# Performance work log

Measured on AMD Instinct MI355X. Metric: run time of the kernel, lower is better.

Reference implementation:

```python
import jax, jax.numpy as jnp
import numpy as np

NUM_ITERATIONS = 3


def _squash_elementwise(s):
    # Faithful to original: squared_norm summed over trailing axis of size 1
    # => elementwise squash v = s^2 * s / ((1 + s^2) * sqrt(s^2))
    sq = s * s
    return sq * s / ((1.0 + sq) * jnp.sqrt(sq))


def setup_inputs() -> dict:
    key = jax.random.key(0)
    k1, k2 = jax.random.split(key)
    B, R, C, O, I = 256, 1152, 10, 16, 8
    x = jax.random.normal(k1, (B, R, I), dtype=jnp.float32)
    W = jax.random.normal(k2, (R, C, O, I), dtype=jnp.float32)
    return {"x": x, "W": W}


def reference(x, W):
    # x: (B, R, I); W: (R, C, O, I)
    R, C, O, I = W.shape
    # u_hat[b,r,c,o] = sum_i W[r,c,o,i] * x[b,r,i]   (matmul W @ x per route/capsule)
    u_hat = jnp.einsum('rcoi,bri->brco', W, x)  # (B, R, C, O)
    b_ij = jnp.zeros((R, C), dtype=x.dtype)  # batch-shared routing logits
    v = None
    for it in range(NUM_ITERATIONS):
        c_ij = jax.nn.softmax(b_ij, axis=0)  # softmax over routes (dim=1 in torch)
        s_j = jnp.einsum('rc,brco->bco', c_ij, u_hat)  # weighted sum over routes
        v = _squash_elementwise(s_j)  # (B, C, O)
        if it < NUM_ITERATIONS - 1:
            # agreement a[b,r,c] = u_hat[b,r,c,:] . v[b,c,:]
            a_ij = jnp.einsum('brco,bco->brc', u_hat, v)
            b_ij = b_ij + a_ij.mean(axis=0)  # mean over batch, batch-shared update
    return v[..., None]  # (B, C, O, 1) matches v_j.squeeze(1)
```

## Files before the change

### kernel.cpp

```cpp
#include <hip/hip_runtime.h>

static constexpr int B_ = 256;
static constexpr int R_ = 1152;
static constexpr int C_ = 10;
static constexpr int O_ = 16;
static constexpr int I_ = 8;
static constexpr int SCO = C_ * O_;
static constexpr int K_ = R_ * I_;
static constexpr int NB = 256;

typedef short bf16x8 __attribute__((ext_vector_type(8)));
typedef float f32x4  __attribute__((ext_vector_type(4)));

__device__ __forceinline__ unsigned short f2bf(float f) {
  union { float f; unsigned int u; } c; c.f = f;
  const unsigned int u = c.u;
  return (unsigned short)((u + 0x7fffu + ((u >> 16) & 1u)) >> 16);
}
__device__ __forceinline__ float bf2f(unsigned short h) {
  union { unsigned int u; float f; } c; c.u = ((unsigned int)h) << 16; return c.f;
}

#define FLAG_IDX(b)    ((b) * 16)
#define REQ_IDX(k)     (4096 + (k) * 16)
#define ACK_IDX(e)     (4224 + ((e) - 1) * 16)
#define GO_IDX(k)      (4352 + (k) * 16)
#define RESP_IDX(e, x) (4480 + (((e) - 1) * 8 + (x)) * 16)
#define NBLK_IDX(x)    (5120 + (x) * 16)

__device__ __forceinline__ void gsync(unsigned int* bar, unsigned int epoch,
                                      unsigned int myxcd) {
  __syncthreads();
  const int bx = blockIdx.x, t = threadIdx.x;
  if (bx == 0) {
    if (t == 0)
      __hip_atomic_store(&bar[FLAG_IDX(0)], epoch,
                         __ATOMIC_RELAXED, __HIP_MEMORY_SCOPE_AGENT);
    if (t < 256) {
      int guard = 0;
      while (__hip_atomic_load(&bar[FLAG_IDX(t)],
                               __ATOMIC_RELAXED, __HIP_MEMORY_SCOPE_AGENT) < epoch) {
        __builtin_amdgcn_s_sleep(4);
        if (++guard > (1 << 18)) break;
      }
    }
    __syncthreads();
    if (t == 0) {
      for (int k2 = 0; k2 < 8; ++k2)
        __hip_atomic_store(&bar[REQ_IDX(k2)], epoch,
                           __ATOMIC_RELAXED, __HIP_MEMORY_SCOPE_AGENT);
      const unsigned oldr = __hip_atomic_fetch_add(&bar[RESP_IDX(epoch, myxcd)], 1u,
                              __ATOMIC_RELAXED, __HIP_MEMORY_SCOPE_AGENT);
      if (oldr == 0)
        __hip_atomic_fetch_add(&bar[ACK_IDX(epoch)], 1u,
                               __ATOMIC_RELEASE, __HIP_MEMORY_SCOPE_AGENT);
      unsigned nx = 0;
      for (int x2 = 0; x2 < 8; ++x2)
        nx += (__hip_atomic_load(&bar[NBLK_IDX(x2)],
                 __ATOMIC_RELAXED, __HIP_MEMORY_SCOPE_AGENT) > 0u) ? 1u : 0u;
      int guard = 0;
      while (__hip_atomic_load(&bar[ACK_IDX(epoch)],
                               __ATOMIC_RELAXED, __HIP_MEMORY_SCOPE_AGENT) < nx) {
        __builtin_amdgcn_s_sleep(4);
        if (++guard > (1 << 18)) break;
      }
      __builtin_amdgcn_fence(__ATOMIC_RELEASE, "agent");
      for (int k2 = 0; k2 < 8; ++k2)
        __hip_atomic_store(&bar[GO_IDX(k2)], epoch,
                           __ATOMIC_RELAXED, __HIP_MEMORY_SCOPE_AGENT);
    }
  } else {
    if (t == 0) {
      __hip_atomic_store(&bar[FLAG_IDX(bx)], epoch,
                         __ATOMIC_RELAXED, __HIP_MEMORY_SCOPE_AGENT);
      unsigned int* rq = &bar[REQ_IDX(bx & 7)];
      int guard = 0;
      while (__hip_atomic_load(rq, __ATOMIC_RELAXED,
                               __HIP_MEMORY_SCOPE_AGENT) < epoch) {
        __builtin_amdgcn_s_sleep(8);
        if (++guard > (1 << 17)) break;
      }
      const unsigned oldr = __hip_atomic_fetch_add(&bar[RESP_IDX(epoch, myxcd)], 1u,
                              __ATOMIC_RELAXED, __HIP_MEMORY_SCOPE_AGENT);
      if (oldr == 0)
        __hip_atomic_fetch_add(&bar[ACK_IDX(epoch)], 1u,
                               __ATOMIC_RELEASE, __HIP_MEMORY_SCOPE_AGENT);
      unsigned int* g = &bar[GO_IDX(bx & 7)];
      guard = 0;
      while (__hip_atomic_load(g, __ATOMIC_RELAXED,
                               __HIP_MEMORY_SCOPE_AGENT) < epoch) {
        __builtin_amdgcn_s_sleep(16);
        if (++guard > (1 << 17)) break;
      }
    }
  }
  __syncthreads();
  asm volatile("" ::: "memory");
}

__device__ __forceinline__ void gemm_phase(
    int git, const unsigned short* __restrict__ xb,
    const unsigned short* __restrict__ wraw, const float* __restrict__ eX,
    float* __restrict__ Z, unsigned short* __restrict__ vbw,
    float* __restrict__ out, unsigned char* smem,
    int bx, int t, int w, int mrow, int quad) {
  float* sred = (float*)smem;
  float* szed = (float*)(smem + 16384);
  float* e_lds = (float*)(smem + 20480);
  const int xcd = bx & 7, j = bx >> 3;
  const int mtile = (xcd >> 1) * 4 + j / 5;
  const int c = (xcd & 1) * 5 + j % 5;
  const int m0 = mtile * 16;
  if (git > 0) {
    for (int idx = t; idx < 1152; idx += 512) e_lds[idx] = eX[c * 1152 + idx];
    if (t < 10) szed[t] = atomicAdd(&Z[git * 10 + t], 0.0f);
    __syncthreads();
  }
  const unsigned short* ap = xb + (size_t)(m0 + mrow) * K_ + w * 1152 + quad * 8;
  const unsigned short* bp = wraw + ((size_t)(w * 144 + quad) * C_ + c) * 128 + mrow * 8;
  f32x4 acc = {0.0f, 0.0f, 0.0f, 0.0f};
  if (git == 0) {
#pragma unroll 6
    for (int kk = 0; kk < 36; ++kk) {
      const bf16x8 a = *(const bf16x8*)(ap + kk * 32);
      const bf16x8 b = *(const bf16x8*)(bp + (size_t)kk * 5120);
      acc = __builtin_amdgcn_mfma_f32_16x16x32_bf16(a, b, acc, 0, 0, 0);
    }
  } else {
#pragma unroll 6
    for (int kk = 0; kk < 36; ++kk) {
      const bf16x8 a = *(const bf16x8*)(ap + kk * 32);
      const bf16x8 braw = *(const bf16x8*)(bp + (size_t)kk * 5120);
      const float ev = e_lds[w * 144 + kk * 4 + quad];
      bf16x8 b;
#pragma unroll
      for (int j8 = 0; j8 < 8; ++j8)
        b[j8] = (short)f2bf(bf2f((unsigned short)braw[j8]) * ev);
      acc = __builtin_amdgcn_mfma_f32_16x16x32_bf16(a, b, acc, 0, 0, 0);
    }
  }
#pragma unroll
  for (int rg = 0; rg < 4; ++rg)
    sred[w * 272 + mrow * 17 + quad * 4 + rg] = acc[rg];
  __syncthreads();
  if (t < 256) {
    int m, n;
    if (git == 2) { m = t >> 4; n = t & 15; } else { n = t >> 4; m = t & 15; }
    const int e = n * 17 + m;
    const float ss = ((sred[0 * 272 + e] + sred[1 * 272 + e]) +
                      (sred[2 * 272 + e] + sred[3 * 272 + e])) +
                     ((sred[4 * 272 + e] + sred[5 * 272 + e]) +
                      (sred[6 * 272 + e] + sred[7 * 272 + e]));
    const float s = (git == 0) ? ss * (1.0f / 1152.0f) : ss / szed[c];
    const float v = s * fabsf(s) / (1.0f + s * s);
    if (git == 2) out[(size_t)(m0 + m) * SCO + c * 16 + n] = v;
    else          vbw[(size_t)(c * 16 + n) * 256 + m0 + m] = f2bf(v);
  }
}

__device__ __forceinline__ void pv_phase(
    int it, const unsigned short* __restrict__ xT,
    const unsigned short* __restrict__ vbr, const float* __restrict__ W,
    float* __restrict__ bvec, float* __restrict__ eOut, float* __restrict__ Z,
    unsigned char* smem, int bx, int t, int w, int mrow, int quad) {
  unsigned short* svb = (unsigned short*)smem;
  float* sp = (float*)smem;
  float* sbs = (float*)(smem + 81920);
  const int seg = (bx & 7) * 18 + (bx >> 3);
  const int r0 = seg * 8;
  bf16x8 afr[8];
  if (w < 4) {
    const unsigned short* ap = xT + (size_t)(seg * 64 + w * 16 + mrow) * 256 + quad * 8;
#pragma unroll
    for (int kk = 0; kk < 8; ++kk) afr[kk] = *(const bf16x8*)(ap + kk * 32);
  }
  {
    const char* src = (const char*)vbr;
    char* dst = (char*)svb;
#pragma unroll
    for (int i = 0; i < 10; ++i) {
      const int ci = i * 512 + t;
      const int lin = ci * 16;
      const int n = ci >> 5;
      *(bf16x8*)(dst + (lin ^ ((n & 7) << 4))) = *(const bf16x8*)(src + lin);
    }
  }
  __syncthreads();
  f32x4 acc[10];
  if (w < 4) {
#pragma unroll
    for (int c = 0; c < 10; ++c) acc[c] = (f32x4){0.0f, 0.0f, 0.0f, 0.0f};
#pragma unroll
    for (int c = 0; c < 10; ++c) {
      const int n = c * 16 + mrow;
      const int base = n * 512 + quad * 16;
#pragma unroll
      for (int kk = 0; kk < 8; ++kk) {
        const bf16x8 b = *(const bf16x8*)((const char*)svb +
                          ((base + kk * 64) ^ ((n & 7) << 4)));
        acc[c] = __builtin_amdgcn_mfma_f32_16x16x32_bf16(afr[kk], b, acc[c], 0, 0, 0);
      }
    }
  }
  __syncthreads();
  if (w < 4) {
#pragma unroll
    for (int c = 0; c < 10; ++c)
#pragma unroll
      for (int rg = 0; rg < 4; ++rg) {
        const int ml = w * 16 + quad * 4 + rg;
        sp[(c * 8 + (ml >> 3)) * 128 + mrow * 8 + (ml & 7)] = acc[c][rg];
      }
  }
  __syncthreads();
  const int p16 = t >> 5, l32 = t & 31;
#pragma unroll
  for (int ch = 0; ch < 5; ++ch) {
    const int pair = ch * 16 + p16;
    const int rl = pair / 10, c = pair - rl * 10;
    const float4 pv4 = *(const float4*)&sp[(c * 8 + rl) * 128 + l32 * 4];
    const float4 wv = *(const float4*)(W + (size_t)(r0 + rl) * 1280 + c * 128 + l32 * 4);
    float prod = wv.x * pv4.x + wv.y * pv4.y + wv.z * pv4.z + wv.w * pv4.w;
    prod += __shfl_xor(prod, 1);  prod += __shfl_xor(prod, 2);
    prod += __shfl_xor(prod, 4);  prod += __shfl_xor(prod, 8);
    prod += __shfl_xor(prod, 16);
    if (l32 == 0) sbs[rl * 10 + c] = prod;
  }
  __syncthreads();
  if (t < 80) {
    const int rl = t / 10, c = t - rl * 10;
    const int r = r0 + rl;
    float b = sbs[t] * (1.0f / 256.0f);
    if (it != 0) b += bvec[r * C_ + c];
    bvec[r * C_ + c] = b;
    const float e = expf(b);
    sbs[t] = e;
    eOut[c * 1152 + r] = e;
  }
  __syncthreads();
  if (t < 10) {
    float z = 0.0f;
#pragma unroll
    for (int rl = 0; rl < 8; ++rl) z += sbs[rl * 10 + t];
    atomicAdd(&Z[(it + 1) * 10 + t], z);
  }
}

__global__ __launch_bounds__(512, 1) void mega(
    const float* __restrict__ x, const float* __restrict__ W,
    float* __restrict__ out, unsigned int* __restrict__ bar,
    float* __restrict__ bvec, float* __restrict__ Z,
    float* __restrict__ eA, float* __restrict__ eB,
    unsigned short* __restrict__ xb, unsigned short* __restrict__ wraw,
    unsigned short* __restrict__ xT,
    unsigned short* __restrict__ vb0, unsigned short* __restrict__ vb1) {
  __shared__ __align__(16) unsigned char smem[82560];
  const int bx = blockIdx.x;
  const int t = threadIdx.x;
  const int lane = t & 63;
  const int w = __builtin_amdgcn_readfirstlane(t >> 6);
  const int mrow = lane & 15, quad = lane >> 4;

  unsigned int myxcd;
  asm volatile("s_getreg_b32 %0, hwreg(HW_REG_XCC_ID)" : "=s"(myxcd));
  myxcd &= 7u;
  if (t == 0)
    __hip_atomic_fetch_add(&bar[NBLK_IDX(myxcd)], 1u,
                           __ATOMIC_RELAXED, __HIP_MEMORY_SCOPE_AGENT);
  if (bx == 0 && t < 32) Z[t] = 0.0f;

  {
    const float4* wf = (const float4*)W;
    ushort4* wr = (ushort4*)wraw;
    for (int idx = t; idx < 1440; idx += 512) {
      const int j = bx * 1440 + idx;
      const float4 v4 = wf[j];
      ushort4 r4;
      r4.x = f2bf(v4.x); r4.y = f2bf(v4.y); r4.z = f2bf(v4.z); r4.w = f2bf(v4.w);
      wr[j] = r4;
    }
    float* sx = (float*)smem;
    const int bq = bx & 3, rseg = bx >> 2;
    const int rbase = rseg * 18;
    for (int idx = t; idx < 64 * 36; idx += 512) {
      const int b = idx / 36, f4 = idx - b * 36;
      const size_t off = (size_t)(bq * 64 + b) * K_ + rbase * I_ + f4 * 4;
      const float4 val = *(const float4*)(x + off);
      ushort4 o4;
      o4.x = f2bf(val.x); o4.y = f2bf(val.y); o4.z = f2bf(val.z); o4.w = f2bf(val.w);
      *(ushort4*)(xb + off) = o4;
      const int rr = f4 >> 1, i4 = (f4 & 1) * 4;
      sx[(rr * 8 + i4 + 0) * 68 + b] = val.x;
      sx[(rr * 8 + i4 + 1) * 68 + b] = val.y;
      sx[(rr * 8 + i4 + 2) * 68 + b] = val.z;
      sx[(rr * 8 + i4 + 3) * 68 + b] = val.w;
    }
    __syncthreads();
    for (int row = w * 18; row < w * 18 + 18; ++row)
      xT[(size_t)(rseg * 144 + row) * 256 + bq * 64 + lane] = f2bf(sx[row * 68 + lane]);
  }
  gsync(bar, 1, myxcd);

  if (bx < 160) gemm_phase(0, xb, wraw, nullptr, Z, vb0, out, smem, bx, t, w, mrow, quad);
  gsync(bar, 2, myxcd);

  if (bx < 144) pv_phase(0, xT, vb0, W, bvec, eA, Z, smem, bx, t, w, mrow, quad);
  gsync(bar, 3, myxcd);

  if (bx < 160) gemm_phase(1, xb, wraw, eA, Z, vb1, out, smem, bx, t, w, mrow, quad);
  gsync(bar, 4, myxcd);

  if (bx < 144) pv_phase(1, xT, vb1, W, bvec, eB, Z, smem, bx, t, w, mrow, quad);
  gsync(bar, 5, myxcd);

  if (bx < 160) gemm_phase(2, xb, wraw, eB, Z, nullptr, out, smem, bx, t, w, mrow, quad);
}

extern "C" void kernel_launch(void* const* d_in, const int* in_sizes, int n_in,
                              void* d_out, int out_size, void* d_ws, size_t ws_size,
                              hipStream_t stream) {
  const float* x = (const float*)d_in[0];
  const float* W = (const float*)d_in[1];
  float* out = (float*)d_out;

  unsigned int* bar = (unsigned int*)d_ws;
  float* bvec = (float*)d_ws + 5376;
  float* Z    = bvec + R_ * C_;
  float* eA   = Z + 32;
  float* eB   = eA + C_ * R_;
  unsigned short* xb   = (unsigned short*)(eB + C_ * R_);
  unsigned short* wraw = xb + (size_t)B_ * K_;
  unsigned short* xT   = wraw + (size_t)R_ * C_ * O_ * I_;
  unsigned short* vb0  = xT + (size_t)R_ * 8 * 256;
  unsigned short* vb1  = vb0 + (size_t)160 * 256;

  hipMemsetAsync(bar, 0, 21504, stream);
  mega<<<NB, 512, 0, stream>>>(x, W, out, bar, bvec, Z, eA, eB,
                               xb, wraw, xT, vb0, vb1);
}
```

Measured before the change: 136.9 us.

## Fuse first routing GEMM into conversion phase to remove one grid barrier

Blocks 0-159 now compute the first iteration's weighted sum straight from the fp32 inputs, converting to bf16 in registers. The remaining 96 blocks do the W/x bf16 conversion and the x transpose in a strided loop. This removes one grid-wide barrier and one full phase, and the gemm phase becomes branch-free because the git==0 special case is gone. The cost is a conversion load that now sits on fewer blocks, fp32 reads of x and W twice, and a shorter go-flag sleep in the barrier spin.

```diff
diff --git a/kernel.cpp b/kernel.cpp
--- a/kernel.cpp
+++ b/kernel.cpp
@@ -89,7 +89,7 @@
       guard = 0;
       while (__hip_atomic_load(g, __ATOMIC_RELAXED,
                                __HIP_MEMORY_SCOPE_AGENT) < epoch) {
-        __builtin_amdgcn_s_sleep(16);
+        __builtin_amdgcn_s_sleep(8);
         if (++guard > (1 << 17)) break;
       }
     }
@@ -111,33 +111,22 @@
   const int mtile = (xcd >> 1) * 4 + j / 5;
   const int c = (xcd & 1) * 5 + j % 5;
   const int m0 = mtile * 16;
-  if (git > 0) {
-    for (int idx = t; idx < 1152; idx += 512) e_lds[idx] = eX[c * 1152 + idx];
-    if (t < 10) szed[t] = atomicAdd(&Z[git * 10 + t], 0.0f);
-    __syncthreads();
-  }
+  for (int idx = t; idx < 1152; idx += 512) e_lds[idx] = eX[c * 1152 + idx];
+  if (t < 10) szed[t] = atomicAdd(&Z[git * 10 + t], 0.0f);
+  __syncthreads();
   const unsigned short* ap = xb + (size_t)(m0 + mrow) * K_ + w * 1152 + quad * 8;
   const unsigned short* bp = wraw + ((size_t)(w * 144 + quad) * C_ + c) * 128 + mrow * 8;
   f32x4 acc = {0.0f, 0.0f, 0.0f, 0.0f};
-  if (git == 0) {
 #pragma unroll 6
-    for (int kk = 0; kk < 36; ++kk) {
-      const bf16x8 a = *(const bf16x8*)(ap + kk * 32);
-      const bf16x8 b = *(const bf16x8*)(bp + (size_t)kk * 5120);
-      acc = __builtin_amdgcn_mfma_f32_16x16x32_bf16(a, b, acc, 0, 0, 0);
-    }
-  } else {
-#pragma unroll 6
-    for (int kk = 0; kk < 36; ++kk) {
-      const bf16x8 a = *(const bf16x8*)(ap + kk * 32);
-      const bf16x8 braw = *(const bf16x8*)(bp + (size_t)kk * 5120);
-      const float ev = e_lds[w * 144 + kk * 4 + quad];
-      bf16x8 b;
-#pragma unroll
-      for (int j8 = 0; j8 < 8; ++j8)
-        b[j8] = (short)f2bf(bf2f((unsigned short)braw[j8]) * ev);
-      acc = __builtin_amdgcn_mfma_f32_16x16x32_bf16(a, b, acc, 0, 0, 0);
-    }
+  for (int kk = 0; kk < 36; ++kk) {
+    const bf16x8 a = *(const bf16x8*)(ap + kk * 32);
+    const bf16x8 braw = *(const bf16x8*)(bp + (size_t)kk * 5120);
+    const float ev = e_lds[w * 144 + kk * 4 + quad];
+    bf16x8 b;
+#pragma unroll
+    for (int j8 = 0; j8 < 8; ++j8)
+      b[j8] = (short)f2bf(bf2f((unsigned short)braw[j8]) * ev);
+    acc = __builtin_amdgcn_mfma_f32_16x16x32_bf16(a, b, acc, 0, 0, 0);
   }
 #pragma unroll
   for (int rg = 0; rg < 4; ++rg)
@@ -151,7 +140,7 @@
                       (sred[2 * 272 + e] + sred[3 * 272 + e])) +
                      ((sred[4 * 272 + e] + sred[5 * 272 + e]) +
                       (sred[6 * 272 + e] + sred[7 * 272 + e]));
-    const float s = (git == 0) ? ss * (1.0f / 1152.0f) : ss / szed[c];
+    const float s = ss / szed[c];
     const float v = s * fabsf(s) / (1.0f + s * s);
     if (git == 2) out[(size_t)(m0 + m) * SCO + c * 16 + n] = v;
     else          vbw[(size_t)(c * 16 + n) * 256 + m0 + m] = f2bf(v);
@@ -269,49 +258,90 @@
                            __ATOMIC_RELAXED, __HIP_MEMORY_SCOPE_AGENT);
   if (bx == 0 && t < 32) Z[t] = 0.0f;
 
-  {
+  if (bx < 160) {
+    float* sred = (float*)smem;
+    const int xcd = bx & 7, j = bx >> 3;
+    const int mtile = (xcd >> 1) * 4 + j / 5;
+    const int c = (xcd & 1) * 5 + j % 5;
+    const int m0 = mtile * 16;
+    const float* apf = x + (size_t)(m0 + mrow) * K_ + w * 1152 + quad * 8;
+    const float* bpf = W + ((size_t)(w * 144 + quad) * C_ + c) * 128 + mrow * 8;
+    f32x4 acc = {0.0f, 0.0f, 0.0f, 0.0f};
+#pragma unroll 4
+    for (int kk = 0; kk < 36; ++kk) {
+      const float4 a0 = *(const float4*)(apf + kk * 32);
+      const float4 a1 = *(const float4*)(apf + kk * 32 + 4);
+      const float4 b0 = *(const float4*)(bpf + (size_t)kk * 5120);
+      const float4 b1 = *(const float4*)(bpf + (size_t)kk * 5120 + 4);
+      bf16x8 a, b;
+      a[0] = (short)f2bf(a0.x); a[1] = (short)f2bf(a0.y);
+      a[2] = (short)f2bf(a0.z); a[3] = (short)f2bf(a0.w);
+      a[4] = (short)f2bf(a1.x); a[5] = (short)f2bf(a1.y);
+      a[6] = (short)f2bf(a1.z); a[7] = (short)f2bf(a1.w);
+      b[0] = (short)f2bf(b0.x); b[1] = (short)f2bf(b0.y);
+      b[2] = (short)f2bf(b0.z); b[3] = (short)f2bf(b0.w);
+      b[4] = (short)f2bf(b1.x); b[5] = (short)f2bf(b1.y);
+      b[6] = (short)f2bf(b1.z); b[7] = (short)f2bf(b1.w);
+      acc = __builtin_amdgcn_mfma_f32_16x16x32_bf16(a, b, acc, 0, 0, 0);
+    }
+#pragma unroll
+    for (int rg = 0; rg < 4; ++rg)
+      sred[w * 272 + mrow * 17 + quad * 4 + rg] = acc[rg];
+    __syncthreads();
+    if (t < 256) {
+      const int n = t >> 4, m = t & 15;
+      const int e = n * 17 + m;
+      const float ss = ((sred[0 * 272 + e] + sred[1 * 272 + e]) +
+                        (sred[2 * 272 + e] + sred[3 * 272 + e])) +
+                       ((sred[4 * 272 + e] + sred[5 * 272 + e]) +
+                        (sred[6 * 272 + e] + sred[7 * 272 + e]));
+      const float s = ss * (1.0f / 1152.0f);
+      const float v = s * fabsf(s) / (1.0f + s * s);
+      vb0[(size_t)(c * 16 + n) * 256 + m0 + m] = f2bf(v);
+    }
+  } else {
     const float4* wf = (const float4*)W;
     ushort4* wr = (ushort4*)wraw;
-    for (int idx = t; idx < 1440; idx += 512) {
-      const int j = bx * 1440 + idx;
+    for (int idx = t; idx < 3840; idx += 512) {
+      const int j = (bx - 160) * 3840 + idx;
       const float4 v4 = wf[j];
       ushort4 r4;
       r4.x = f2bf(v4.x); r4.y = f2bf(v4.y); r4.z = f2bf(v4.z); r4.w = f2bf(v4.w);
       wr[j] = r4;
     }
     float* sx = (float*)smem;
-    const int bq = bx & 3, rseg = bx >> 2;
-    const int rbase = rseg * 18;
-    for (int idx = t; idx < 64 * 36; idx += 512) {
-      const int b = idx / 36, f4 = idx - b * 36;
-      const size_t off = (size_t)(bq * 64 + b) * K_ + rbase * I_ + f4 * 4;
-      const float4 val = *(const float4*)(x + off);
-      ushort4 o4;
-      o4.x = f2bf(val.x); o4.y = f2bf(val.y); o4.z = f2bf(val.z); o4.w = f2bf(val.w);
-      *(ushort4*)(xb + off) = o4;
-      const int rr = f4 >> 1, i4 = (f4 & 1) * 4;
-      sx[(rr * 8 + i4 + 0) * 68 + b] = val.x;
-      sx[(rr * 8 + i4 + 1) * 68 + b] = val.y;
-      sx[(rr * 8 + i4 + 2) * 68 + b] = val.z;
-      sx[(rr * 8 + i4 + 3) * 68 + b] = val.w;
-    }
-    __syncthreads();
-    for (int row = w * 18; row < w * 18 + 18; ++row)
-      xT[(size_t)(rseg * 144 + row) * 256 + bq * 64 + lane] = f2bf(sx[row * 68 + lane]);
+    for (int u = bx - 160; u < 256; u += 96) {
+      const int bq = u & 3, rseg = u >> 2;
+      const int rbase = rseg * 18;
+      __syncthreads();
+      for (int idx = t; idx < 64 * 36; idx += 512) {
+        const int b = idx / 36, f4 = idx - b * 36;
+        const size_t off = (size_t)(bq * 64 + b) * K_ + rbase * I_ + f4 * 4;
+        const float4 val = *(const float4*)(x + off);
+        ushort4 o4;
+        o4.x = f2bf(val.x); o4.y = f2bf(val.y); o4.z = f2bf(val.z); o4.w = f2bf(val.w);
+        *(ushort4*)(xb + off) = o4;
+        const int rr = f4 >> 1, i4 = (f4 & 1) * 4;
+        sx[(rr * 8 + i4 + 0) * 68 + b] = val.x;
+        sx[(rr * 8 + i4 + 1) * 68 + b] = val.y;
+        sx[(rr * 8 + i4 + 2) * 68 + b] = val.z;
+        sx[(rr * 8 + i4 + 3) * 68 + b] = val.w;
+      }
+      __syncthreads();
+      for (int row = w * 18; row < w * 18 + 18; ++row)
+        xT[(size_t)(rseg * 144 + row) * 256 + bq * 64 + lane] = f2bf(sx[row * 68 + lane]);
+    }
   }
   gsync(bar, 1, myxcd);
 
-  if (bx < 160) gemm_phase(0, xb, wraw, nullptr, Z, vb0, out, smem, bx, t, w, mrow, quad);
+  if (bx < 144) pv_phase(0, xT, vb0, W, bvec, eA, Z, smem, bx, t, w, mrow, quad);
   gsync(bar, 2, myxcd);
 
-  if (bx < 144) pv_phase(0, xT, vb0, W, bvec, eA, Z, smem, bx, t, w, mrow, quad);
+  if (bx < 160) gemm_phase(1, xb, wraw, eA, Z, vb1, out, smem, bx, t, w, mrow, quad);
   gsync(bar, 3, myxcd);
 
-  if (bx < 160) gemm_phase(1, xb, wraw, eA, Z, vb1, out, smem, bx, t, w, mrow, quad);
+  if (bx < 144) pv_phase(1, xT, vb1, W, bvec, eB, Z, smem, bx, t, w, mrow, quad);
   gsync(bar, 4, myxcd);
-
-  if (bx < 144) pv_phase(1, xT, vb1, W, bvec, eB, Z, smem, bx, t, w, mrow, quad);
-  gsync(bar, 5, myxcd);
 
   if (bx < 160) gemm_phase(2, xb, wraw, eB, Z, nullptr, out, smem, bx, t, w, mrow, quad);
 }
```

Result: no change. 137.2 us (+0.2%).
